# Kernel optimization log

Hardware: AMD Instinct MI355X
Metric: run time of the kernel (lower is better)

## Reference

```python
import jax, jax.numpy as jnp
import numpy as np

N = 4096      # nodes
IN = 512      # in_dim
HID = 64      # hid_dim
OUT = 8       # out_dim (classes)
H = 2         # num_heads / meta-paths
SEM = 32      # semantic attention hidden size
P_EDGE = 0.005  # edge probability -> avg degree ~20


def setup_inputs() -> dict:
    key = jax.random.key(0)
    ks = jax.random.split(key, 12)
    h = jax.random.normal(ks[0], (N, IN), jnp.float32)
    # sparse binary adjacency per head, with self-loops (densified as in adj.to_dense())
    adj = (jax.random.uniform(ks[1], (H, N, N)) < P_EDGE).astype(jnp.float32)
    adj = jnp.clip(adj + jnp.eye(N, dtype=jnp.float32)[None], 0.0, 1.0)
    sc = lambda k, s: (jax.random.normal(k, s, jnp.float32) * 0.05)
    W1 = sc(ks[2], (H, IN, HID))
    b1 = jnp.zeros((H, HID), jnp.float32)
    Wq = sc(ks[3], (H, HID, HID)); bq = jnp.zeros((H, HID), jnp.float32)
    Wk = sc(ks[4], (H, HID, HID)); bk = jnp.zeros((H, HID), jnp.float32)
    Wv = sc(ks[5], (H, HID, HID)); bv = jnp.zeros((H, HID), jnp.float32)
    sem_W1 = sc(ks[6], (HID, SEM)); sem_b1 = jnp.zeros((SEM,), jnp.float32)
    sem_W2 = sc(ks[7], (SEM, 1))
    pred_W = sc(ks[8], (HID, OUT)); pred_b = jnp.zeros((OUT,), jnp.float32)
    return dict(h=h, adj=adj, W1=W1, b1=b1, Wq=Wq, bq=bq, Wk=Wk, bk=bk,
                Wv=Wv, bv=bv, sem_W1=sem_W1, sem_b1=sem_b1, sem_W2=sem_W2,
                pred_W=pred_W, pred_b=pred_b)


def reference(h, adj, W1, b1, Wq, bq, Wk, bk, Wv, bv,
              sem_W1, sem_b1, sem_W2, pred_W, pred_b):
    def embed(adj_i, W1_i, b1_i, Wq_i, bq_i, Wk_i, bk_i, Wv_i, bv_i):
        # GraphConvolution (Kipf): adj @ (h @ W) + b, then ReLU
        x = jax.nn.relu(adj_i @ (h @ W1_i) + b1_i)            # [N, HID]
        Q = x @ Wq_i + bq_i
        K = x @ Wk_i + bk_i
        V = x @ Wv_i + bv_i
        # dense-masked attention: adj.to_dense() * (Q K^T), softmax over rows
        A_tilde = adj_i * (Q @ K.T)                            # [N, N]
        att = jax.nn.softmax(A_tilde, axis=1)
        # gcn_norm: symmetric D^{-1/2} A D^{-1/2}, degree = row sums
        d = att.sum(axis=1)
        dinv = jnp.where(d > 0, jax.lax.rsqrt(d), 0.0)
        att_n = dinv[:, None] * att * dinv[None, :]
        return jax.nn.relu(att_n @ V)                          # [N, HID]

    z = jax.vmap(embed)(adj, W1, b1, Wq, bq, Wk, bk, Wv, bv)   # [H, N, HID]
    z = jnp.transpose(z, (1, 0, 2))                            # [N, H, HID]
    # SemanticAttention: project -> mean over nodes -> softmax over dim=1
    w = jnp.tanh(z @ sem_W1 + sem_b1) @ sem_W2                 # [N, H, 1]
    w = w.mean(axis=0)                                         # [H, 1]
    beta = jax.nn.softmax(w, axis=1)  # faithful to torch.softmax(w, dim=1)
    p2 = (beta[None] * z).sum(axis=1)                          # [N, HID]
    return jax.nn.softmax(p2 @ pred_W + pred_b, axis=1)        # [N, OUT]
```

## Files before the change

### kernel.cpp

```cpp
#include <hip/hip_runtime.h>
#include <hip/hip_bf16.h>

#define NN   4096
#define IND  512
#define HIDD 64
#define OUTD 8
#define NH   2
#define CAP  128

using bf16 = __hip_bfloat16;

__device__ __forceinline__ float b2f(bf16 v) { return __bfloat162float(v); }

__global__ void k_sniff(const unsigned* __restrict__ aw, int* __restrict__ flag) {
    __shared__ int s;
    if (threadIdx.x == 0) s = 0;
    __syncthreads();
    for (int i = threadIdx.x; i < 256; i += 64)
        if ((aw[(size_t)i * 4097] & 0xFFFFu) == 0x3F80u) atomicOr(&s, 1);
    __syncthreads();
    if (threadIdx.x == 0) *flag = s;
}

#define OFF_H   0
#define OFF_W1  2097152
#define OFF_B1  2162688
#define OFF_WQ  2162816
#define OFF_BQ  2171008
#define OFF_WK  2171136
#define OFF_BK  2179328
#define OFF_WV  2179456
#define OFF_BV  2187648
#define OFF_PW  2187776
#define OFF_PB  2188288
#define CONV_TOTAL 2188296

struct ConvArgs { const void* s[11]; };

__global__ void __launch_bounds__(256) k_conv(ConvArgs a, const int* __restrict__ flag,
                                              float* __restrict__ dst) {
    const int cum[12] = {OFF_H, OFF_W1, OFF_B1, OFF_WQ, OFF_BQ, OFF_WK, OFF_BK,
                         OFF_WV, OFF_BV, OFF_PW, OFF_PB, CONV_TOTAL};
    int isbf = *flag;
    int g = blockIdx.x * 256 + threadIdx.x;
    if (g >= CONV_TOTAL) return;
    int seg = 0;
    while (seg < 10 && g >= cum[seg + 1]) ++seg;
    int off = g - cum[seg];
    float v = isbf ? b2f(((const bf16*)a.s[seg])[off]) : ((const float*)a.s[seg])[off];
    dst[g] = v;
}

__global__ void __launch_bounds__(256) k_csr(const void* __restrict__ adjv,
                                             const int* __restrict__ flag,
                                             int* __restrict__ deg,
                                             int* __restrict__ cols) {
    int row = blockIdx.x;
    __shared__ int cnt;
    __shared__ int lc[CAP];
    if (threadIdx.x == 0) cnt = 0;
    __syncthreads();
    if (*flag) {
        const uint4* a4 = reinterpret_cast<const uint4*>((const bf16*)adjv + (size_t)row * NN);
#pragma unroll
        for (int it = 0; it < 2; ++it) {
            int v = threadIdx.x + it * 256;
            uint4 d = a4[v];
            unsigned u[4] = {d.x, d.y, d.z, d.w};
            int base = v * 8;
#pragma unroll
            for (int w = 0; w < 4; ++w) {
                if (u[w] & 0xFFFFu) { int p = atomicAdd(&cnt, 1); if (p < CAP) lc[p] = base + 2 * w; }
                if (u[w] >> 16)     { int p = atomicAdd(&cnt, 1); if (p < CAP) lc[p] = base + 2 * w + 1; }
            }
        }
    } else {
        const uint4* a4 = reinterpret_cast<const uint4*>((const float*)adjv + (size_t)row * NN);
#pragma unroll
        for (int it = 0; it < 4; ++it) {
            int v = threadIdx.x + it * 256;
            uint4 d = a4[v];
            unsigned u[4] = {d.x, d.y, d.z, d.w};
            int base = v * 4;
#pragma unroll
            for (int w = 0; w < 4; ++w) {
                if (u[w]) { int p = atomicAdd(&cnt, 1); if (p < CAP) lc[p] = base + w; }
            }
        }
    }
    __syncthreads();
    int c = cnt; if (c > CAP) c = CAP;
    if (threadIdx.x == 0) deg[row] = c;
    int* oc = cols + (size_t)row * CAP;
    for (int k = threadIdx.x; k < c; k += 256) oc[k] = lc[k];
}

__device__ __forceinline__ void gemm64_body(const float* __restrict__ A, int lda, int Ka,
                                            const float* __restrict__ B,
                                            const float* __restrict__ bias,
                                            float* __restrict__ C, int i0) {
    __shared__ __align__(16) float As[32][68];
    __shared__ __align__(16) float Bs[32][68];
    int tid = threadIdx.x;
    int r0 = (tid >> 4) * 4;
    int c0 = (tid & 15) * 4;
    float acc[4][4] = {};
    for (int kc = 0; kc < Ka; kc += 32) {
        {
            int row = tid >> 2;
            int kp  = (tid & 3) * 8;
            const float* p = A + (size_t)(i0 + row) * lda + kc + kp;
            float4 a = *reinterpret_cast<const float4*>(p);
            float4 b = *reinterpret_cast<const float4*>(p + 4);
            float t8[8] = {a.x, a.y, a.z, a.w, b.x, b.y, b.z, b.w};
#pragma unroll
            for (int j = 0; j < 8; ++j) As[kp + j][row] = t8[j];
        }
        {
            int kb = tid >> 3;
            int cp = (tid & 7) * 8;
            const float* p = B + (size_t)(kc + kb) * HIDD + cp;
            float4 a = *reinterpret_cast<const float4*>(p);
            float4 b = *reinterpret_cast<const float4*>(p + 4);
            float t8[8] = {a.x, a.y, a.z, a.w, b.x, b.y, b.z, b.w};
#pragma unroll
            for (int j = 0; j < 8; ++j) Bs[kb][cp + j] = t8[j];
        }
        __syncthreads();
#pragma unroll 8
        for (int k = 0; k < 32; ++k) {
            float4 av = *reinterpret_cast<const float4*>(&As[k][r0]);
            float4 bv = *reinterpret_cast<const float4*>(&Bs[k][c0]);
            float aa[4] = {av.x, av.y, av.z, av.w};
            float bb[4] = {bv.x, bv.y, bv.z, bv.w};
#pragma unroll
            for (int ia = 0; ia < 4; ++ia)
#pragma unroll
                for (int ib = 0; ib < 4; ++ib)
                    acc[ia][ib] = fmaf(aa[ia], bb[ib], acc[ia][ib]);
        }
        __syncthreads();
    }
    float bv[4] = {0.f, 0.f, 0.f, 0.f};
    if (bias) {
#pragma unroll
        for (int b = 0; b < 4; ++b) bv[b] = bias[c0 + b];
    }
#pragma unroll
    for (int ia = 0; ia < 4; ++ia)
#pragma unroll
        for (int ib = 0; ib < 4; ++ib)
            C[(size_t)(i0 + r0 + ia) * HIDD + c0 + ib] = acc[ia][ib] + bv[ib];
}

__global__ void __launch_bounds__(256) k_hw(const float* __restrict__ p32,
                                            float* __restrict__ hW) {
    int head = blockIdx.y;
    gemm64_body(p32 + OFF_H, IND, IND, p32 + OFF_W1 + (size_t)head * IND * HIDD, nullptr,
                hW + (size_t)head * NN * HIDD, blockIdx.x * 64);
}

__global__ void __launch_bounds__(256) k_qkv(const float* __restrict__ x,
                                             const float* __restrict__ p32,
                                             float* Q, float* K, float* V) {
    int head = blockIdx.y, z = blockIdx.z;
    const float* W  = p32 + ((z == 0) ? OFF_WQ : (z == 1) ? OFF_WK : OFF_WV) + (size_t)head * HIDD * HIDD;
    const float* bb = p32 + ((z == 0) ? OFF_BQ : (z == 1) ? OFF_BK : OFF_BV) + (size_t)head * HIDD;
    float* C        = (z == 0) ? Q  : (z == 1) ? K  : V;
    gemm64_body(x + (size_t)head * NN * HIDD, HIDD, HIDD, W, bb,
                C + (size_t)head * NN * HIDD, blockIdx.x * 64);
}

__global__ void k_aggx(const float* __restrict__ hW, const float* __restrict__ p32,
                       const int* __restrict__ deg, const int* __restrict__ cols,
                       float* __restrict__ x, float* __restrict__ vsum) {
    int h = blockIdx.y;
    int i = blockIdx.x * 4 + threadIdx.y;
    int t = threadIdx.x;
    if (blockIdx.x == 0 && blockIdx.y == 0) {
        int tid = threadIdx.y * 64 + threadIdx.x;
        if (tid < NH * HIDD) vsum[tid] = 0.f;
    }
    const float* hWh = hW + (size_t)h * NN * HIDD;
    int r = h * NN + i;
    int d = deg[r];
    const int* cl = cols + (size_t)r * CAP;
    float acc = p32[OFF_B1 + h * HIDD + t];
    for (int e = 0; e < d; ++e) acc += hWh[(size_t)cl[e] * HIDD + t];
    x[(size_t)r * HIDD + t] = fmaxf(acc, 0.f);
}

__global__ void k_vsum(const float* __restrict__ V, float* __restrict__ vsum) {
    int h = blockIdx.x, chunk = blockIdx.y, t = threadIdx.x;
    const float* Vh = V + (size_t)h * NN * HIDD;
    float a = 0.f;
    int i0 = chunk * 128;
    for (int i = i0; i < i0 + 128; ++i) a += Vh[(size_t)i * HIDD + t];
    atomicAdd(&vsum[h * HIDD + t], a);
}

__global__ void __launch_bounds__(64) k_attn(const float* __restrict__ Q,
                                             const float* __restrict__ Km,
                                             const float* __restrict__ V,
                                             const float* __restrict__ vsum,
                                             const int* __restrict__ deg,
                                             const int* __restrict__ cols,
                                             const float* __restrict__ p32,
                                             const int* __restrict__ flag,
                                             void* __restrict__ outv) {
    int i = blockIdx.x;
    int t = threadIdx.x;
    __shared__ __align__(16) float qs[HIDD];
    __shared__ float wgt[CAP];
    __shared__ int   cs[CAP];
    __shared__ float p2s[HIDD];
    float p2 = 0.f;

    for (int h = 0; h < NH; ++h) {
        int r = h * NN + i;
        int d = deg[r];
        const int* cl   = cols + (size_t)r * CAP;
        const float* Qh = Q + (size_t)h * NN * HIDD;
        const float* Kh = Km + (size_t)h * NN * HIDD;
        const float* Vh = V + (size_t)h * NN * HIDD;
        __syncthreads();
        qs[t] = Qh[(size_t)i * HIDD + t];
        for (int e = t; e < d; e += 64) cs[e] = cl[e];
        __syncthreads();

        float s0 = 0.f, s1 = 0.f;
        float lmax = 0.f;
        const float4* q4 = reinterpret_cast<const float4*>(qs);
        if (t < d) {
            const float4* K4 = reinterpret_cast<const float4*>(Kh + (size_t)cs[t] * HIDD);
            float s = 0.f;
#pragma unroll 4
            for (int k = 0; k < 16; ++k) {
                float4 kv = K4[k]; float4 qv = q4[k];
                s += qv.x * kv.x + qv.y * kv.y + qv.z * kv.z + qv.w * kv.w;
            }
            s0 = s; lmax = fmaxf(lmax, s);
        }
        if (t + 64 < d) {
            const float4* K4 = reinterpret_cast<const float4*>(Kh + (size_t)cs[t + 64] * HIDD);
            float s = 0.f;
#pragma unroll 4
            for (int k = 0; k < 16; ++k) {
                float4 kv = K4[k]; float4 qv = q4[k];
                s += qv.x * kv.x + qv.y * kv.y + qv.z * kv.z + qv.w * kv.w;
            }
            s1 = s; lmax = fmaxf(lmax, s);
        }
#pragma unroll
        for (int off = 32; off; off >>= 1) lmax = fmaxf(lmax, __shfl_xor(lmax, off));
        float m  = lmax;
        float eb = __expf(-m);
        float lsum = 0.f;
        if (t < d)      { float w = __expf(s0 - m); lsum += w; wgt[t] = w - eb; }
        if (t + 64 < d) { float w = __expf(s1 - m); lsum += w; wgt[t + 64] = w - eb; }
#pragma unroll
        for (int off = 32; off; off >>= 1) lsum += __shfl_xor(lsum, off);
        float Z = lsum + (float)(NN - d) * eb;
        float c = 1.f / Z;
        __syncthreads();

        float acc = eb * vsum[h * HIDD + t];
        for (int e = 0; e < d; ++e) acc += wgt[e] * Vh[(size_t)cs[e] * HIDD + t];
        p2 += fmaxf(acc * c, 0.f);
    }

    p2s[t] = p2;
    __syncthreads();
    if (t < OUTD) {
        float a = p32[OFF_PB + t];
#pragma unroll 8
        for (int k = 0; k < HIDD; ++k) a += p2s[k] * p32[OFF_PW + k * OUTD + t];
        float mx = a;
#pragma unroll
        for (int off = 4; off; off >>= 1) mx = fmaxf(mx, __shfl_xor(mx, off));
        float e = __expf(a - mx);
        float s = e;
#pragma unroll
        for (int off = 4; off; off >>= 1) s += __shfl_xor(s, off);
        float v = e / s;
        if (*flag) ((bf16*)outv)[(size_t)i * OUTD + t] = __float2bfloat16(v);
        else       ((float*)outv)[(size_t)i * OUTD + t] = v;
    }
}

extern "C" void kernel_launch(void* const* d_in, const int* in_sizes, int n_in,
                              void* d_out, int out_size, void* d_ws, size_t ws_size,
                              hipStream_t stream) {
    const void* adj = d_in[1];

    char* w = (char*)d_ws;
    int*   flag = (int*)w;                        w += 256;
    float* p32  = (float*)w;                      w += (size_t)CONV_TOTAL * 4;
    int*   deg  = (int*)w;                        w += (size_t)NH * NN * 4;
    int*   cols = (int*)w;                        w += (size_t)NH * NN * CAP * 4;
    float* hW   = (float*)w;                      w += (size_t)NH * NN * HIDD * 4;
    float* x    = (float*)w;                      w += (size_t)NH * NN * HIDD * 4;
    float* Q    = (float*)w;                      w += (size_t)NH * NN * HIDD * 4;
    float* K    = (float*)w;                      w += (size_t)NH * NN * HIDD * 4;
    float* V    = (float*)w;                      w += (size_t)NH * NN * HIDD * 4;
    float* vsum = (float*)w;                      w += (size_t)NH * HIDD * 4;

    ConvArgs ca;
    ca.s[0] = d_in[0];
    ca.s[1] = d_in[2];
    ca.s[2] = d_in[3];
    ca.s[3] = d_in[4];
    ca.s[4] = d_in[5];
    ca.s[5] = d_in[6];
    ca.s[6] = d_in[7];
    ca.s[7] = d_in[8];
    ca.s[8] = d_in[9];
    ca.s[9] = d_in[13];
    ca.s[10] = d_in[14];

    k_sniff<<<1, 64, 0, stream>>>((const unsigned*)adj, flag);
    k_conv <<<(CONV_TOTAL + 255) / 256, 256, 0, stream>>>(ca, flag, p32);
    k_csr  <<<NH * NN, 256, 0, stream>>>(adj, flag, deg, cols);
    k_hw   <<<dim3(NN / 64, NH), 256, 0, stream>>>(p32, hW);
    k_aggx <<<dim3(NN / 4, NH), dim3(64, 4), 0, stream>>>(hW, p32, deg, cols, x, vsum);
    k_qkv  <<<dim3(NN / 64, NH, 3), 256, 0, stream>>>(x, p32, Q, K, V);
    k_vsum <<<dim3(NH, 32), 64, 0, stream>>>(V, vsum);
    k_attn <<<NN, 64, 0, stream>>>(Q, K, V, vsum, deg, cols, p32, flag, d_out);
}
```

Before: 311.1 us.

## Drop sniff/convert kernels, fuse V column-sum into QKV, pack four nodes per attention block

```diff
diff --git a/kernel.cpp b/kernel.cpp
--- a/kernel.cpp
+++ b/kernel.cpp
@@ -12,55 +12,47 @@
 
 __device__ __forceinline__ float b2f(bf16 v) { return __bfloat162float(v); }
 
-__global__ void k_sniff(const unsigned* __restrict__ aw, int* __restrict__ flag) {
-    __shared__ int s;
-    if (threadIdx.x == 0) s = 0;
-    __syncthreads();
-    for (int i = threadIdx.x; i < 256; i += 64)
-        if ((aw[(size_t)i * 4097] & 0xFFFFu) == 0x3F80u) atomicOr(&s, 1);
-    __syncthreads();
-    if (threadIdx.x == 0) *flag = s;
-}
-
-#define OFF_H   0
-#define OFF_W1  2097152
-#define OFF_B1  2162688
-#define OFF_WQ  2162816
-#define OFF_BQ  2171008
-#define OFF_WK  2171136
-#define OFF_BK  2179328
-#define OFF_WV  2179456
-#define OFF_BV  2187648
-#define OFF_PW  2187776
-#define OFF_PB  2188288
-#define CONV_TOTAL 2188296
-
-struct ConvArgs { const void* s[11]; };
-
-__global__ void __launch_bounds__(256) k_conv(ConvArgs a, const int* __restrict__ flag,
-                                              float* __restrict__ dst) {
-    const int cum[12] = {OFF_H, OFF_W1, OFF_B1, OFF_WQ, OFF_BQ, OFF_WK, OFF_BK,
-                         OFF_WV, OFF_BV, OFF_PW, OFF_PB, CONV_TOTAL};
-    int isbf = *flag;
-    int g = blockIdx.x * 256 + threadIdx.x;
-    if (g >= CONV_TOTAL) return;
-    int seg = 0;
-    while (seg < 10 && g >= cum[seg + 1]) ++seg;
-    int off = g - cum[seg];
-    float v = isbf ? b2f(((const bf16*)a.s[seg])[off]) : ((const float*)a.s[seg])[off];
-    dst[g] = v;
+__device__ __forceinline__ bool sniff_bf(const unsigned* __restrict__ adjw) {
+    return (adjw[0] & 0xFFFFu) == 0x3F80u;
+}
+__device__ __forceinline__ float ldf(const void* p, int i, bool isbf) {
+    return isbf ? b2f(((const bf16*)p)[i]) : ((const float*)p)[i];
+}
+__device__ __forceinline__ void load8f(const void* p, size_t off, bool isbf, float* o) {
+    if (isbf) {
+        uint4 d = *reinterpret_cast<const uint4*>((const bf16*)p + off);
+        unsigned u[4] = {d.x, d.y, d.z, d.w};
+#pragma unroll
+        for (int w = 0; w < 4; ++w) {
+            o[2 * w]     = __uint_as_float(u[w] << 16);
+            o[2 * w + 1] = __uint_as_float(u[w] & 0xFFFF0000u);
+        }
+    } else {
+        const float* q = (const float*)p + off;
+        float4 a = *reinterpret_cast<const float4*>(q);
+        float4 b = *reinterpret_cast<const float4*>(q + 4);
+        o[0] = a.x; o[1] = a.y; o[2] = a.z; o[3] = a.w;
+        o[4] = b.x; o[5] = b.y; o[6] = b.z; o[7] = b.w;
+    }
+}
+__device__ __forceinline__ void load8_f32(const float* q, float* o) {
+    float4 a = *reinterpret_cast<const float4*>(q);
+    float4 b = *reinterpret_cast<const float4*>(q + 4);
+    o[0] = a.x; o[1] = a.y; o[2] = a.z; o[3] = a.w;
+    o[4] = b.x; o[5] = b.y; o[6] = b.z; o[7] = b.w;
 }
 
 __global__ void __launch_bounds__(256) k_csr(const void* __restrict__ adjv,
-                                             const int* __restrict__ flag,
                                              int* __restrict__ deg,
-                                             int* __restrict__ cols) {
+                                             int* __restrict__ cols,
+                                             float* __restrict__ vsum) {
+    if (blockIdx.x == 0 && threadIdx.x < NH * HIDD) vsum[threadIdx.x] = 0.f;
     int row = blockIdx.x;
     __shared__ int cnt;
     __shared__ int lc[CAP];
     if (threadIdx.x == 0) cnt = 0;
     __syncthreads();
-    if (*flag) {
+    if (sniff_bf((const unsigned*)adjv)) {
         const uint4* a4 = reinterpret_cast<const uint4*>((const bf16*)adjv + (size_t)row * NN);
 #pragma unroll
         for (int it = 0; it < 2; ++it) {
@@ -95,34 +87,31 @@
     for (int k = threadIdx.x; k < c; k += 256) oc[k] = lc[k];
 }
 
-__device__ __forceinline__ void gemm64_body(const float* __restrict__ A, int lda, int Ka,
-                                            const float* __restrict__ B,
-                                            const float* __restrict__ bias,
-                                            float* __restrict__ C, int i0) {
+template <typename T>
+__device__ __forceinline__ void hw_body(const T* __restrict__ A,
+                                        const T* __restrict__ B,
+                                        float* __restrict__ C, int i0) {
     __shared__ __align__(16) float As[32][68];
     __shared__ __align__(16) float Bs[32][68];
     int tid = threadIdx.x;
     int r0 = (tid >> 4) * 4;
     int c0 = (tid & 15) * 4;
     float acc[4][4] = {};
-    for (int kc = 0; kc < Ka; kc += 32) {
+    for (int kc = 0; kc < IND; kc += 32) {
         {
             int row = tid >> 2;
             int kp  = (tid & 3) * 8;
-            const float* p = A + (size_t)(i0 + row) * lda + kc + kp;
-            float4 a = *reinterpret_cast<const float4*>(p);
-            float4 b = *reinterpret_cast<const float4*>(p + 4);
-            float t8[8] = {a.x, a.y, a.z, a.w, b.x, b.y, b.z, b.w};
+            float t8[8];
+            load8f((const void*)A, (size_t)(i0 + row) * IND + kc + kp,
+                   sizeof(T) == 2, t8);
 #pragma unroll
             for (int j = 0; j < 8; ++j) As[kp + j][row] = t8[j];
         }
         {
             int kb = tid >> 3;
             int cp = (tid & 7) * 8;
-            const float* p = B + (size_t)(kc + kb) * HIDD + cp;
-            float4 a = *reinterpret_cast<const float4*>(p);
-            float4 b = *reinterpret_cast<const float4*>(p + 4);
-            float t8[8] = {a.x, a.y, a.z, a.w, b.x, b.y, b.z, b.w};
+            float t8[8];
+            load8f((const void*)B, (size_t)(kc + kb) * HIDD + cp, sizeof(T) == 2, t8);
 #pragma unroll
             for (int j = 0; j < 8; ++j) Bs[kb][cp + j] = t8[j];
         }
@@ -141,79 +130,142 @@
         }
         __syncthreads();
     }
-    float bv[4] = {0.f, 0.f, 0.f, 0.f};
-    if (bias) {
-#pragma unroll
-        for (int b = 0; b < 4; ++b) bv[b] = bias[c0 + b];
-    }
 #pragma unroll
     for (int ia = 0; ia < 4; ++ia)
-#pragma unroll
-        for (int ib = 0; ib < 4; ++ib)
-            C[(size_t)(i0 + r0 + ia) * HIDD + c0 + ib] = acc[ia][ib] + bv[ib];
-}
-
-__global__ void __launch_bounds__(256) k_hw(const float* __restrict__ p32,
+        *reinterpret_cast<float4*>(C + (size_t)(i0 + r0 + ia) * HIDD + c0) =
+            make_float4(acc[ia][0], acc[ia][1], acc[ia][2], acc[ia][3]);
+}
+
+__global__ void __launch_bounds__(256) k_hw(const void* __restrict__ h,
+                                            const void* __restrict__ W1,
+                                            const unsigned* __restrict__ adjw,
                                             float* __restrict__ hW) {
     int head = blockIdx.y;
-    gemm64_body(p32 + OFF_H, IND, IND, p32 + OFF_W1 + (size_t)head * IND * HIDD, nullptr,
-                hW + (size_t)head * NN * HIDD, blockIdx.x * 64);
-}
-
-__global__ void __launch_bounds__(256) k_qkv(const float* __restrict__ x,
-                                             const float* __restrict__ p32,
-                                             float* Q, float* K, float* V) {
-    int head = blockIdx.y, z = blockIdx.z;
-    const float* W  = p32 + ((z == 0) ? OFF_WQ : (z == 1) ? OFF_WK : OFF_WV) + (size_t)head * HIDD * HIDD;
-    const float* bb = p32 + ((z == 0) ? OFF_BQ : (z == 1) ? OFF_BK : OFF_BV) + (size_t)head * HIDD;
-    float* C        = (z == 0) ? Q  : (z == 1) ? K  : V;
-    gemm64_body(x + (size_t)head * NN * HIDD, HIDD, HIDD, W, bb,
-                C + (size_t)head * NN * HIDD, blockIdx.x * 64);
-}
-
-__global__ void k_aggx(const float* __restrict__ hW, const float* __restrict__ p32,
+    float* Ch = hW + (size_t)head * NN * HIDD;
+    if (sniff_bf(adjw))
+        hw_body<bf16>((const bf16*)h, (const bf16*)W1 + (size_t)head * IND * HIDD, Ch, blockIdx.x * 64);
+    else
+        hw_body<float>((const float*)h, (const float*)W1 + (size_t)head * IND * HIDD, Ch, blockIdx.x * 64);
+}
+
+__global__ void k_aggx(const float* __restrict__ hW, const void* __restrict__ b1,
+                       const unsigned* __restrict__ adjw,
                        const int* __restrict__ deg, const int* __restrict__ cols,
-                       float* __restrict__ x, float* __restrict__ vsum) {
+                       float* __restrict__ x) {
+    bool isbf = sniff_bf(adjw);
     int h = blockIdx.y;
     int i = blockIdx.x * 4 + threadIdx.y;
     int t = threadIdx.x;
-    if (blockIdx.x == 0 && blockIdx.y == 0) {
-        int tid = threadIdx.y * 64 + threadIdx.x;
-        if (tid < NH * HIDD) vsum[tid] = 0.f;
-    }
     const float* hWh = hW + (size_t)h * NN * HIDD;
     int r = h * NN + i;
     int d = deg[r];
     const int* cl = cols + (size_t)r * CAP;
-    float acc = p32[OFF_B1 + h * HIDD + t];
+    float acc = ldf(b1, h * HIDD + t, isbf);
     for (int e = 0; e < d; ++e) acc += hWh[(size_t)cl[e] * HIDD + t];
     x[(size_t)r * HIDD + t] = fmaxf(acc, 0.f);
 }
 
-__global__ void k_vsum(const float* __restrict__ V, float* __restrict__ vsum) {
-    int h = blockIdx.x, chunk = blockIdx.y, t = threadIdx.x;
-    const float* Vh = V + (size_t)h * NN * HIDD;
-    float a = 0.f;
-    int i0 = chunk * 128;
-    for (int i = i0; i < i0 + 128; ++i) a += Vh[(size_t)i * HIDD + t];
-    atomicAdd(&vsum[h * HIDD + t], a);
-}
-
-__global__ void __launch_bounds__(64) k_attn(const float* __restrict__ Q,
-                                             const float* __restrict__ Km,
-                                             const float* __restrict__ V,
-                                             const float* __restrict__ vsum,
-                                             const int* __restrict__ deg,
-                                             const int* __restrict__ cols,
-                                             const float* __restrict__ p32,
-                                             const int* __restrict__ flag,
-                                             void* __restrict__ outv) {
-    int i = blockIdx.x;
-    int t = threadIdx.x;
-    __shared__ __align__(16) float qs[HIDD];
-    __shared__ float wgt[CAP];
-    __shared__ int   cs[CAP];
-    __shared__ float p2s[HIDD];
+__global__ void __launch_bounds__(256) k_qkv(const float* __restrict__ x,
+                                             const void* Wq, const void* bq,
+                                             const void* Wk, const void* bk,
+                                             const void* Wv, const void* bv,
+                                             const unsigned* __restrict__ adjw,
+                                             float* Q, float* K, float* V,
+                                             float* __restrict__ vsum) {
+    bool isbf = sniff_bf(adjw);
+    int head = blockIdx.y, z = blockIdx.z;
+    int i0 = blockIdx.x * 64;
+    const void* W  = (z == 0) ? Wq : (z == 1) ? Wk : Wv;
+    const void* bb = (z == 0) ? bq : (z == 1) ? bk : bv;
+    float* C       = ((z == 0) ? Q : (z == 1) ? K : V) + (size_t)head * NN * HIDD;
+    const float* xh = x + (size_t)head * NN * HIDD;
+
+    __shared__ __align__(16) float As[64][68];
+    __shared__ __align__(16) float Bs[64][68];
+    int tid = threadIdx.x;
+    {
+        int row = tid >> 2;
+        int kp  = (tid & 3) * 16;
+        float t8[8];
+        load8_f32(xh + (size_t)(i0 + row) * HIDD + kp, t8);
+#pragma unroll
+        for (int j = 0; j < 8; ++j) As[kp + j][row] = t8[j];
+        load8_f32(xh + (size_t)(i0 + row) * HIDD + kp + 8, t8);
+#pragma unroll
+        for (int j = 0; j < 8; ++j) As[kp + 8 + j][row] = t8[j];
+    }
+    {
+        int kb = tid >> 2;
+        int cp = (tid & 3) * 16;
+        size_t base = (size_t)head * HIDD * HIDD + (size_t)kb * HIDD + cp;
+        float t8[8];
+        load8f(W, base, isbf, t8);
+#pragma unroll
+        for (int j = 0; j < 8; ++j) Bs[kb][cp + j] = t8[j];
+        load8f(W, base + 8, isbf, t8);
+#pragma unroll
+        for (int j = 0; j < 8; ++j) Bs[kb][cp + 8 + j] = t8[j];
+    }
+    __syncthreads();
+
+    int r0 = (tid >> 4) * 4;
+    int c0 = (tid & 15) * 4;
+    float acc[4][4] = {};
+#pragma unroll 8
+    for (int k = 0; k < 64; ++k) {
+        float4 av = *reinterpret_cast<const float4*>(&As[k][r0]);
+        float4 bv4 = *reinterpret_cast<const float4*>(&Bs[k][c0]);
+        float aa[4] = {av.x, av.y, av.z, av.w};
+        float bbv[4] = {bv4.x, bv4.y, bv4.z, bv4.w};
+#pragma unroll
+        for (int ia = 0; ia < 4; ++ia)
+#pragma unroll
+            for (int ib = 0; ib < 4; ++ib)
+                acc[ia][ib] = fmaf(aa[ia], bbv[ib], acc[ia][ib]);
+    }
+    float bz[4];
+#pragma unroll
+    for (int b = 0; b < 4; ++b) bz[b] = ldf(bb, head * HIDD + c0 + b, isbf);
+#pragma unroll
+    for (int ia = 0; ia < 4; ++ia)
+        *reinterpret_cast<float4*>(C + (size_t)(i0 + r0 + ia) * HIDD + c0) =
+            make_float4(acc[ia][0] + bz[0], acc[ia][1] + bz[1],
+                        acc[ia][2] + bz[2], acc[ia][3] + bz[3]);
+
+    if (z == 2) {
+        float vpart[4];
+#pragma unroll
+        for (int ib = 0; ib < 4; ++ib)
+            vpart[ib] = acc[0][ib] + acc[1][ib] + acc[2][ib] + acc[3][ib] + 64.f / 64.f * 0.f;
+        __syncthreads();
+        if (tid < HIDD) As[0][tid] = 0.f;
+        __syncthreads();
+#pragma unroll
+        for (int ib = 0; ib < 4; ++ib)
+            atomicAdd(&As[0][c0 + ib], vpart[ib] + 16.f * bz[ib]);
+        __syncthreads();
+        if (tid < HIDD) atomicAdd(&vsum[head * HIDD + tid], As[0][tid]);
+    }
+}
+
+__global__ void __launch_bounds__(256) k_attn(const float* __restrict__ Q,
+                                              const float* __restrict__ Km,
+                                              const float* __restrict__ V,
+                                              const float* __restrict__ vsum,
+                                              const int* __restrict__ deg,
+                                              const int* __restrict__ cols,
+                                              const void* __restrict__ predW,
+                                              const void* __restrict__ predb,
+                                              const unsigned* __restrict__ adjw,
+                                              void* __restrict__ outv) {
+    bool isbf = sniff_bf(adjw);
+    int wid = threadIdx.x >> 6;
+    int t   = threadIdx.x & 63;
+    int i   = blockIdx.x * 4 + wid;
+    __shared__ __align__(16) float qs[4][64];
+    __shared__ float wgt[4][CAP];
+    __shared__ int   cs[4][CAP];
+    __shared__ float p2s[4][64];
     float p2 = 0.f;
 
     for (int h = 0; h < NH; ++h) {
@@ -223,16 +275,14 @@
         const float* Qh = Q + (size_t)h * NN * HIDD;
         const float* Kh = Km + (size_t)h * NN * HIDD;
         const float* Vh = V + (size_t)h * NN * HIDD;
-        __syncthreads();
-        qs[t] = Qh[(size_t)i * HIDD + t];
-        for (int e = t; e < d; e += 64) cs[e] = cl[e];
-        __syncthreads();
+        qs[wid][t] = Qh[(size_t)i * HIDD + t];
+        for (int e = t; e < d; e += 64) cs[wid][e] = cl[e];
 
         float s0 = 0.f, s1 = 0.f;
         float lmax = 0.f;
-        const float4* q4 = reinterpret_cast<const float4*>(qs);
+        const float4* q4 = reinterpret_cast<const float4*>(qs[wid]);
         if (t < d) {
-            const float4* K4 = reinterpret_cast<const float4*>(Kh + (size_t)cs[t] * HIDD);
+            const float4* K4 = reinterpret_cast<const float4*>(Kh + (size_t)cs[wid][t] * HIDD);
             float s = 0.f;
 #pragma unroll 4
             for (int k = 0; k < 16; ++k) {
@@ -242,7 +292,7 @@
             s0 = s; lmax = fmaxf(lmax, s);
         }
         if (t + 64 < d) {
-            const float4* K4 = reinterpret_cast<const float4*>(Kh + (size_t)cs[t + 64] * HIDD);
+            const float4* K4 = reinterpret_cast<const float4*>(Kh + (size_t)cs[wid][t + 64] * HIDD);
             float s = 0.f;
 #pragma unroll 4
             for (int k = 0; k < 16; ++k) {
@@ -256,25 +306,23 @@
         float m  = lmax;
         float eb = __expf(-m);
         float lsum = 0.f;
-        if (t < d)      { float w = __expf(s0 - m); lsum += w; wgt[t] = w - eb; }
-        if (t + 64 < d) { float w = __expf(s1 - m); lsum += w; wgt[t + 64] = w - eb; }
+        if (t < d)      { float w = __expf(s0 - m); lsum += w; wgt[wid][t] = w - eb; }
+        if (t + 64 < d) { float w = __expf(s1 - m); lsum += w; wgt[wid][t + 64] = w - eb; }
 #pragma unroll
         for (int off = 32; off; off >>= 1) lsum += __shfl_xor(lsum, off);
         float Z = lsum + (float)(NN - d) * eb;
         float c = 1.f / Z;
-        __syncthreads();
 
         float acc = eb * vsum[h * HIDD + t];
-        for (int e = 0; e < d; ++e) acc += wgt[e] * Vh[(size_t)cs[e] * HIDD + t];
+        for (int e = 0; e < d; ++e) acc += wgt[wid][e] * Vh[(size_t)cs[wid][e] * HIDD + t];
         p2 += fmaxf(acc * c, 0.f);
     }
 
-    p2s[t] = p2;
-    __syncthreads();
+    p2s[wid][t] = p2;
     if (t < OUTD) {
-        float a = p32[OFF_PB + t];
+        float a = ldf(predb, t, isbf);
 #pragma unroll 8
-        for (int k = 0; k < HIDD; ++k) a += p2s[k] * p32[OFF_PW + k * OUTD + t];
+        for (int k = 0; k < HIDD; ++k) a += p2s[wid][k] * ldf(predW, k * OUTD + t, isbf);
         float mx = a;
 #pragma unroll
         for (int off = 4; off; off >>= 1) mx = fmaxf(mx, __shfl_xor(mx, off));
@@ -283,8 +331,8 @@
 #pragma unroll
         for (int off = 4; off; off >>= 1) s += __shfl_xor(s, off);
         float v = e / s;
-        if (*flag) ((bf16*)outv)[(size_t)i * OUTD + t] = __float2bfloat16(v);
-        else       ((float*)outv)[(size_t)i * OUTD + t] = v;
+        if (isbf) ((bf16*)outv)[(size_t)i * OUTD + t] = __float2bfloat16(v);
+        else      ((float*)outv)[(size_t)i * OUTD + t] = v;
     }
 }
 
@@ -292,10 +340,9 @@
                               void* d_out, int out_size, void* d_ws, size_t ws_size,
                               hipStream_t stream) {
     const void* adj = d_in[1];
+    const unsigned* adjw = (const unsigned*)adj;
 
     char* w = (char*)d_ws;
-    int*   flag = (int*)w;                        w += 256;
-    float* p32  = (float*)w;                      w += (size_t)CONV_TOTAL * 4;
     int*   deg  = (int*)w;                        w += (size_t)NH * NN * 4;
     int*   cols = (int*)w;                        w += (size_t)NH * NN * CAP * 4;
     float* hW   = (float*)w;                      w += (size_t)NH * NN * HIDD * 4;
@@ -305,25 +352,10 @@
     float* V    = (float*)w;                      w += (size_t)NH * NN * HIDD * 4;
     float* vsum = (float*)w;                      w += (size_t)NH * HIDD * 4;
 
-    ConvArgs ca;
-    ca.s[0] = d_in[0];
-    ca.s[1] = d_in[2];
-    ca.s[2] = d_in[3];
-    ca.s[3] = d_in[4];
-    ca.s[4] = d_in[5];
-    ca.s[5] = d_in[6];
-    ca.s[6] = d_in[7];
-    ca.s[7] = d_in[8];
-    ca.s[8] = d_in[9];
-    ca.s[9] = d_in[13];
-    ca.s[10] = d_in[14];
-
-    k_sniff<<<1, 64, 0, stream>>>((const unsigned*)adj, flag);
-    k_conv <<<(CONV_TOTAL + 255) / 256, 256, 0, stream>>>(ca, flag, p32);
-    k_csr  <<<NH * NN, 256, 0, stream>>>(adj, flag, deg, cols);
-    k_hw   <<<dim3(NN / 64, NH), 256, 0, stream>>>(p32, hW);
-    k_aggx <<<dim3(NN / 4, NH), dim3(64, 4), 0, stream>>>(hW, p32, deg, cols, x, vsum);
-    k_qkv  <<<dim3(NN / 64, NH, 3), 256, 0, stream>>>(x, p32, Q, K, V);
-    k_vsum <<<dim3(NH, 32), 64, 0, stream>>>(V, vsum);
-    k_attn <<<NN, 64, 0, stream>>>(Q, K, V, vsum, deg, cols, p32, flag, d_out);
-}
+    k_csr <<<NH * NN, 256, 0, stream>>>(adj, deg, cols, vsum);
+    k_hw  <<<dim3(NN / 64, NH), 256, 0, stream>>>(d_in[0], d_in[2], adjw, hW);
+    k_aggx<<<dim3(NN / 4, NH), dim3(64, 4), 0, stream>>>(hW, d_in[3], adjw, deg, cols, x);
+    k_qkv <<<dim3(NN / 64, NH, 3), 256, 0, stream>>>(x, d_in[4], d_in[5], d_in[6], d_in[7],
+                                                     d_in[8], d_in[9], adjw, Q, K, V, vsum);
+    k_attn<<<NN / 4, 256, 0, stream>>>(Q, K, V, vsum, deg, cols, d_in[13], d_in[14], adjw, d_out);
+}
```

After: 292.4 us. 6.0% less time.
